# Kernel tuning notes

Hardware: AMD Instinct MI355X
Metric: run time of the kernel (lower is better)

The kernel has to match this reference:

```python
import jax, jax.numpy as jnp
import numpy as np

# module hyperparameters (from init_kwargs)
K = 32          # out_channels / features per branch
THRESH = 20.0   # firing threshold
KWTA = 4        # winners per branch
RF = 512        # rf_size (number of branches)
L = 2048        # receptive-field length
T = 32          # timesteps (leading 'batch' dim in SpykeTorch)
C = 1           # in_channels


def setup_inputs() -> dict:
    key = jax.random.key(0)
    k1, k2, k3 = jax.random.split(key, 3)
    rec_field = jax.random.uniform(k1, (T, C, RF, L), dtype=jnp.float32)
    W = jax.random.normal(k2, (RF, K, C, L), dtype=jnp.float32)  # per-branch local-conv weights
    reward = jax.random.normal(k3, (1, 1, RF), dtype=jnp.float32)
    return {"rec_field": rec_field, "W": W, "reward": reward}


def _winner_mask(thr, spikes):
    """SpykeTorch sf.get_k_winners for a single branch with 1x1 spatial output.
    thr, spikes: (T, K) thresholded potentials and their sign (0/1).
    Returns a (K,) 0/1 mask over the kwta winning features.
    Score = earliest-spike-dominant total potential, exactly as in SpykeTorch:
      first  = T - sum_t spikes           (first spike time, clamped)
      values = thr[first, k]
      total  = sum_t (spikes*values + spikes * max(spikes*values)*T)
    With 1x1 spatial, inhibition_radius has no effect; picking then zeroing a
    feature == distinct top-k over features with a nonzero check.
    """
    first = jnp.clip((T - spikes.sum(0)).astype(jnp.int32), 0, T - 1)          # (K,)
    vals_at_first = jnp.take_along_axis(thr, first[None, :], axis=0)[0]        # (K,)
    trunc = spikes * vals_at_first[None, :]                                    # (T, K)
    v = trunc.max() * T
    total = (trunc + spikes * v).sum(0)                                        # (K,)
    top_vals, top_idx = jax.lax.top_k(total, KWTA)
    valid = (top_vals != 0).astype(thr.dtype)
    return jnp.zeros((K,), thr.dtype).at[top_idx].max(valid)


def reference(rec_field, W, reward):
    # per-branch local convolution: kernel covers the whole (1,L) input -> 1x1 output
    pot = jnp.einsum('tcrl,rkcl->rtk', rec_field, W)        # (RF, T, K)
    # sf.fire: keep potentials strictly above threshold (F.threshold semantics)
    thr = jnp.where(pot > THRESH, pot, jnp.zeros((), pot.dtype))
    spikes = jnp.sign(thr)
    # kWTA winner masks per branch (coefs), then masked sign
    mask = jax.vmap(_winner_mask)(thr, spikes)              # (RF, K)
    out = jnp.sign(thr * mask[:, None, :])                  # (RF, T, K)
    # torch: cat(dim=2) -> (T,K,RF,1) -> squeeze -> (T,K,RF) -> unsqueeze(1) -> (T,1,K,RF)
    return jnp.transpose(out, (1, 2, 0))[:, None, :, :]
```

## Files before the change

kernel.cpp:

```cpp
#include <hip/hip_runtime.h>
#include <cstdint>


typedef float vf4 __attribute__((ext_vector_type(4)));

#define RFN 512
#define TN  32
#define KN  32
#define LN  2048
#define SPLIT 4
#define LSEG (LN / SPLIT)
#define CHUNK 64
#define NITER (LSEG / CHUNK)

__global__ __launch_bounds__(256, 5) void column1_gemm(
    const float* __restrict__ rec,
    const float* __restrict__ wgt,
    float* __restrict__ wsout)
{
    __shared__ __align__(16) float lds[2 * 64 * CHUNK];
    const int bs   = blockIdx.x;
    const int r    = bs >> 2;
    const int sseg = bs & 3;
    const int l0   = sseg * LSEG;
    const int tid  = threadIdx.x;
    const int lane = tid & 63;
    const int wv   = tid >> 6;
    const int tg   = lane >> 3;
    const int kg   = lane & 7;

    const int c4 = tid & 15;
    const int r0 = tid >> 4;
    const float* gsrc[4];
    int ldoff[4];
#pragma unroll
    for (int s = 0; s < 4; ++s) {
        const int row = r0 + 16 * s;
        const float* g;
        if (row < 32) g = rec + ((size_t)(row * RFN + r)) * LN + l0 + (c4 << 2);
        else          g = wgt + ((size_t)(r * KN + (row - 32))) * LN + l0 + (c4 << 2);
        gsrc[s]  = g;
        ldoff[s] = row * CHUNK + ((c4 ^ (row & 15)) << 2);
    }

    vf4 stage[4];
#pragma unroll
    for (int s = 0; s < 4; ++s)
        stage[s] = __builtin_nontemporal_load((const vf4*)gsrc[s]);

    float acc[4][4];
#pragma unroll
    for (int jt = 0; jt < 4; ++jt)
#pragma unroll
        for (int jk = 0; jk < 4; ++jk) acc[jt][jk] = 0.0f;

    for (int it = 0; it < NITER; ++it) {
        float* buf = lds + (it & 1) * (64 * CHUNK);
#pragma unroll
        for (int s = 0; s < 4; ++s) *(vf4*)(buf + ldoff[s]) = stage[s];
        __syncthreads();
        if (it + 1 < NITER) {
#pragma unroll
            for (int s = 0; s < 4; ++s) {
                gsrc[s] += CHUNK;
                stage[s] = __builtin_nontemporal_load((const vf4*)gsrc[s]);
            }
        }
        const float* rs  = buf;
        const float* wsh = buf + 32 * CHUNK;
#pragma unroll
        for (int q = 0; q < 4; ++q) {
            const int qg = (wv << 2) + q;
            vf4 a[4], b[4];
#pragma unroll
            for (int j = 0; j < 4; ++j) {
                const int row = tg + 8 * j;
                a[j] = *(const vf4*)(rs + row * CHUNK + ((qg ^ (row & 15)) << 2));
            }
#pragma unroll
            for (int j = 0; j < 4; ++j) {
                const int row = kg + 8 * j;
                b[j] = *(const vf4*)(wsh + row * CHUNK + ((qg ^ (row & 15)) << 2));
            }
#pragma unroll
            for (int jt = 0; jt < 4; ++jt)
#pragma unroll
                for (int jk = 0; jk < 4; ++jk) {
                    float v0 = fmaf(a[jt].x, b[jk].x, acc[jt][jk]);
                    v0 = fmaf(a[jt].y, b[jk].y, v0);
                    v0 = fmaf(a[jt].z, b[jk].z, v0);
                    acc[jt][jk] = fmaf(a[jt].w, b[jk].w, v0);
                }
        }
    }

    float* red = lds;
#pragma unroll
    for (int jt = 0; jt < 4; ++jt)
#pragma unroll
        for (int jk = 0; jk < 4; ++jk)
            red[(wv << 10) + (tg + 8 * jt) * 32 + (kg + 8 * jk)] = acc[jt][jk];
    __syncthreads();

    const int o = tid << 2;
    vf4 p0 = *(const vf4*)(red + o);
    vf4 p1 = *(const vf4*)(red + 1024 + o);
    vf4 p2 = *(const vf4*)(red + 2048 + o);
    vf4 p3 = *(const vf4*)(red + 3072 + o);
    vf4 pv = p0 + p1 + p2 + p3;
    *(vf4*)(wsout + (size_t)(r * SPLIT + sseg) * 1024 + o) = pv;
}

__global__ __launch_bounds__(256) void column1_epilogue(
    const float* __restrict__ wsin,
    float* __restrict__ out)
{
    __shared__ float thr_s[32 * 33];
    __shared__ float nspk_s[32], vals_s[32], cand_s[32], tot_s[32], mask_s[32];
    const int r   = blockIdx.x;
    const int tid = threadIdx.x;
    const float* base = wsin + (size_t)r * (SPLIT * 1024);

    const int o = tid << 2;
    vf4 p0 = *(const vf4*)(base + o);
    vf4 p1 = *(const vf4*)(base + 1024 + o);
    vf4 p2 = *(const vf4*)(base + 2048 + o);
    vf4 p3 = *(const vf4*)(base + 3072 + o);
    vf4 ps = p0 + p1 + p2 + p3;
    float pv[4] = { ps.x, ps.y, ps.z, ps.w };
#pragma unroll
    for (int e = 0; e < 4; ++e) {
        const int oo = o + e;
        const float th = (pv[e] > 20.0f) ? pv[e] : 0.0f;
        thr_s[(oo >> 5) * 33 + (oo & 31)] = th;
    }
    __syncthreads();

    if (tid < 32) {
        const int k = tid;
        int ns = 0;
        for (int t = 0; t < 32; ++t) ns += (thr_s[t * 33 + k] > 0.0f) ? 1 : 0;
        int first = 32 - ns; if (first > 31) first = 31;
        const float vf = thr_s[first * 33 + k];
        nspk_s[k] = (float)ns;
        vals_s[k] = vf;
        cand_s[k] = (ns > 0) ? vf : 0.0f;
        mask_s[k] = 0.0f;
    }
    __syncthreads();

    if (tid == 0) {
        float vm = 0.0f;
        for (int k = 0; k < 32; ++k) vm = fmaxf(vm, cand_s[k]);
        const float v = vm * 32.0f;
        for (int k = 0; k < 32; ++k) tot_s[k] = nspk_s[k] * (vals_s[k] + v);
        for (int sel = 0; sel < 4; ++sel) {
            int best = 0; float bv = -1.0f;
            for (int k = 0; k < 32; ++k) {
                const float tv = tot_s[k];
                if (tv > bv) { bv = tv; best = k; }
            }
            if (bv > 0.0f) mask_s[best] = 1.0f;
            tot_s[best] = -1.0f;
        }
    }
    __syncthreads();

#pragma unroll
    for (int e = 0; e < 4; ++e) {
        const int oo = o + e;
        const int t = oo >> 5, k = oo & 31;
        const float v = (thr_s[t * 33 + k] > 0.0f && mask_s[k] > 0.0f) ? 1.0f : 0.0f;
        __builtin_nontemporal_store(v, out + (size_t)t * (KN * RFN) + k * RFN + r);
    }
}

extern "C" void kernel_launch(void* const* d_in, const int* in_sizes, int n_in,
                              void* d_out, int out_size, void* d_ws, size_t ws_size,
                              hipStream_t stream) {
    const float* rec = (const float*)d_in[0];
    const float* wgt = (const float*)d_in[1];
    float* out = (float*)d_out;
    float* ws  = (float*)d_ws;
    column1_gemm<<<dim3(RFN * SPLIT), dim3(256), 0, stream>>>(rec, wgt, ws);
    column1_epilogue<<<dim3(RFN), dim3(256), 0, stream>>>(ws, out);
}
```

Before: 293.8 us.

## Fuse GEMM and kWTA epilogue into one kernel per branch

Removes the split-L partial-sum workspace and the second launch. Each branch is now handled by a single 512-thread block that walks the full receptive field in 128-wide chunks, reduces the eight wave partials in LDS and runs the threshold/winner logic in place. This saves the workspace write and read plus one kernel launch. In exchange there are four times fewer blocks and a 64KB LDS footprint per block, which may cut occupancy and leave the memory-bound loads less latency hiding.

```diff
diff --git a/kernel.cpp b/kernel.cpp
--- a/kernel.cpp
+++ b/kernel.cpp
@@ -3,44 +3,43 @@
 
 
 typedef float vf4 __attribute__((ext_vector_type(4)));
+typedef float vf2 __attribute__((ext_vector_type(2)));
 
 #define RFN 512
 #define TN  32
 #define KN  32
 #define LN  2048
-#define SPLIT 4
-#define LSEG (LN / SPLIT)
-#define CHUNK 64
-#define NITER (LSEG / CHUNK)
+#define CHUNK 128
+#define NITER (LN / CHUNK)
 
-__global__ __launch_bounds__(256, 5) void column1_gemm(
+__global__ __launch_bounds__(512, 4) void column1_fused(
     const float* __restrict__ rec,
     const float* __restrict__ wgt,
-    float* __restrict__ wsout)
+    float* __restrict__ out)
 {
     __shared__ __align__(16) float lds[2 * 64 * CHUNK];
-    const int bs   = blockIdx.x;
-    const int r    = bs >> 2;
-    const int sseg = bs & 3;
-    const int l0   = sseg * LSEG;
+    __shared__ float thr_s[32 * 33];
+    __shared__ float nspk_s[32], vals_s[32], cand_s[32], tot_s[32], mask_s[32];
+
+    const int r    = blockIdx.x;
     const int tid  = threadIdx.x;
     const int lane = tid & 63;
     const int wv   = tid >> 6;
     const int tg   = lane >> 3;
     const int kg   = lane & 7;
 
-    const int c4 = tid & 15;
-    const int r0 = tid >> 4;
+    const int c4 = tid & 31;
+    const int r0 = tid >> 5;
     const float* gsrc[4];
     int ldoff[4];
 #pragma unroll
     for (int s = 0; s < 4; ++s) {
         const int row = r0 + 16 * s;
         const float* g;
-        if (row < 32) g = rec + ((size_t)(row * RFN + r)) * LN + l0 + (c4 << 2);
-        else          g = wgt + ((size_t)(r * KN + (row - 32))) * LN + l0 + (c4 << 2);
+        if (row < 32) g = rec + ((size_t)(row * RFN + r)) * LN + (c4 << 2);
+        else          g = wgt + ((size_t)(r * KN + (row - 32))) * LN + (c4 << 2);
         gsrc[s]  = g;
-        ldoff[s] = row * CHUNK + ((c4 ^ (row & 15)) << 2);
+        ldoff[s] = row * CHUNK + ((c4 ^ (row & 31)) << 2);
     }
 
     vf4 stage[4];
@@ -75,12 +74,12 @@
 #pragma unroll
             for (int j = 0; j < 4; ++j) {
                 const int row = tg + 8 * j;
-                a[j] = *(const vf4*)(rs + row * CHUNK + ((qg ^ (row & 15)) << 2));
+                a[j] = *(const vf4*)(rs + row * CHUNK + ((qg ^ (row & 31)) << 2));
             }
 #pragma unroll
             for (int j = 0; j < 4; ++j) {
                 const int row = kg + 8 * j;
-                b[j] = *(const vf4*)(wsh + row * CHUNK + ((qg ^ (row & 15)) << 2));
+                b[j] = *(const vf4*)(wsh + row * CHUNK + ((qg ^ (row & 31)) << 2));
             }
 #pragma unroll
             for (int jt = 0; jt < 4; ++jt)
@@ -94,6 +93,8 @@
         }
     }
 
+    __syncthreads();
+
     float* red = lds;
 #pragma unroll
     for (int jt = 0; jt < 4; ++jt)
@@ -102,37 +103,18 @@
             red[(wv << 10) + (tg + 8 * jt) * 32 + (kg + 8 * jk)] = acc[jt][jk];
     __syncthreads();
 
-    const int o = tid << 2;
-    vf4 p0 = *(const vf4*)(red + o);
-    vf4 p1 = *(const vf4*)(red + 1024 + o);
-    vf4 p2 = *(const vf4*)(red + 2048 + o);
-    vf4 p3 = *(const vf4*)(red + 3072 + o);
-    vf4 pv = p0 + p1 + p2 + p3;
-    *(vf4*)(wsout + (size_t)(r * SPLIT + sseg) * 1024 + o) = pv;
-}
-
-__global__ __launch_bounds__(256) void column1_epilogue(
-    const float* __restrict__ wsin,
-    float* __restrict__ out)
-{
-    __shared__ float thr_s[32 * 33];
-    __shared__ float nspk_s[32], vals_s[32], cand_s[32], tot_s[32], mask_s[32];
-    const int r   = blockIdx.x;
-    const int tid = threadIdx.x;
-    const float* base = wsin + (size_t)r * (SPLIT * 1024);
-
-    const int o = tid << 2;
-    vf4 p0 = *(const vf4*)(base + o);
-    vf4 p1 = *(const vf4*)(base + 1024 + o);
-    vf4 p2 = *(const vf4*)(base + 2048 + o);
-    vf4 p3 = *(const vf4*)(base + 3072 + o);
-    vf4 ps = p0 + p1 + p2 + p3;
-    float pv[4] = { ps.x, ps.y, ps.z, ps.w };
+    const int o2 = tid << 1;
+    float pv0 = 0.0f, pv1 = 0.0f;
 #pragma unroll
-    for (int e = 0; e < 4; ++e) {
-        const int oo = o + e;
-        const float th = (pv[e] > 20.0f) ? pv[e] : 0.0f;
-        thr_s[(oo >> 5) * 33 + (oo & 31)] = th;
+    for (int s = 0; s < 8; ++s) {
+        vf2 p = *(const vf2*)(red + (s << 10) + o2);
+        pv0 += p.x; pv1 += p.y;
+    }
+    {
+        const float th0 = (pv0 > 20.0f) ? pv0 : 0.0f;
+        const float th1 = (pv1 > 20.0f) ? pv1 : 0.0f;
+        thr_s[(o2 >> 5) * 33 + (o2 & 31)]             = th0;
+        thr_s[((o2 + 1) >> 5) * 33 + ((o2 + 1) & 31)] = th1;
     }
     __syncthreads();
 
@@ -167,8 +149,8 @@
     __syncthreads();
 
 #pragma unroll
-    for (int e = 0; e < 4; ++e) {
-        const int oo = o + e;
+    for (int e = 0; e < 2; ++e) {
+        const int oo = o2 + e;
         const int t = oo >> 5, k = oo & 31;
         const float v = (thr_s[t * 33 + k] > 0.0f && mask_s[k] > 0.0f) ? 1.0f : 0.0f;
         __builtin_nontemporal_store(v, out + (size_t)t * (KN * RFN) + k * RFN + r);
@@ -181,7 +163,5 @@
     const float* rec = (const float*)d_in[0];
     const float* wgt = (const float*)d_in[1];
     float* out = (float*)d_out;
-    float* ws  = (float*)d_ws;
-    column1_gemm<<<dim3(RFN * SPLIT), dim3(256), 0, stream>>>(rec, wgt, ws);
-    column1_epilogue<<<dim3(RFN), dim3(256), 0, stream>>>(ws, out);
+    column1_fused<<<dim3(RFN), dim3(512), 0, stream>>>(rec, wgt, out);
 }
```

Result: faster. 279.7 us (-4.8%).
